# Performance work log

Measured on AMD Instinct MI355X. Metric: run time of the kernel, lower is better.

## Reference

```python
import jax, jax.numpy as jnp
import numpy as np

B, H, S, D = 4, 16, 2048, 64


def setup_inputs() -> dict:
    key = jax.random.key(0)
    kq, kk, kv = jax.random.split(key, 3)
    Q = jax.random.normal(kq, (B, H, S, D), dtype=jnp.float32)
    K = jax.random.normal(kk, (B, H, S, D), dtype=jnp.float32)
    V = jax.random.normal(kv, (B, H, S, D), dtype=jnp.float32)
    # causal mask, broadcasts over (B, H); True = keep, False (==0) = mask out
    mask = jnp.tril(jnp.ones((S, S), dtype=bool))
    return {"Q": Q, "K": K, "V": V, "mask": mask}


def reference(Q, K, V, mask):
    d_k = Q.shape[-1]
    scale = 1.0 / jnp.sqrt(jnp.asarray(d_k, dtype=Q.dtype))
    # [B,H,Sq,Sk] score matrix (the module materializes this fully)
    scores = jnp.einsum('bhqd,bhkd->bhqk', Q, K) * scale
    if mask is not None:
        scores = jnp.where(mask, scores, -jnp.inf)
    attn = jax.nn.softmax(scores, axis=-1)
    return jnp.einsum('bhqk,bhkd->bhqd', attn, V)
```

## Files before the change

kernel.cpp:

```cpp
#include <hip/hip_runtime.h>
#include <math.h>

namespace {

constexpr int SEQ   = 2048;
constexpr int DH    = 64;
constexpr int KVBLK = 64;
constexpr int QW    = 32;
constexpr int NWAVE = 4;
constexpr int QBLK  = QW * NWAVE;
constexpr int NQB   = SEQ / QBLK;
constexpr int BH    = 64;
constexpr int PADB  = 72;

typedef __bf16 bf16x8 __attribute__((ext_vector_type(8)));
typedef float  f32x16 __attribute__((ext_vector_type(16)));

union FragB { bf16x8 v; unsigned u[4]; __bf16 h[8]; };

__device__ __forceinline__ unsigned pack2(float a, float b) {
  unsigned r;
  asm("v_cvt_pk_bf16_f32 %0, %1, %2" : "=v"(r) : "v"(a), "v"(b));
  return r;
}

__device__ __forceinline__ void swap32(int a, int b, int &x, int &y) {
#if __has_builtin(__builtin_amdgcn_permlane32_swap)
  auto r = __builtin_amdgcn_permlane32_swap(a, b, false, false);
  x = r[0]; y = r[1];
#else
  const bool hi = ((threadIdx.x & 63) >= 32);
  const int sa = __shfl_xor(a, 32), sb = __shfl_xor(b, 32);
  x = hi ? sb : a;
  y = hi ? b  : sa;
#endif
}

__device__ __forceinline__ float xhalf_sum(float v) {
  int x, y; swap32(__float_as_int(v), __float_as_int(v), x, y);
  return __int_as_float(x) + __int_as_float(y);
}

__global__ __launch_bounds__(256, 2)
void attn_fwd(const float* __restrict__ Qg, const float* __restrict__ Kg,
              const float* __restrict__ Vg, float* __restrict__ Og)
{
  const int b   = blockIdx.x;
  const int j   = b >> 6;
  const int g   = j >> 2, k = j & 3;
  const int qi  = (g == 0) ? 15 - 2*k
                : (g == 1) ? 2*k
                : (g == 2) ? 14 - 2*k
                :            1 + 2*k;
  const int bh  = (b & 7) + 8 * ((b >> 3) & 7);
  const int qb  = qi * QBLK;
  const int qb64 = qb >> 6;

  const int tid  = threadIdx.x;
  const int wv   = tid >> 6;
  const int lane = tid & 63;
  const int l31  = lane & 31;
  const int hi   = lane >> 5;

  const size_t base = (size_t)bh * SEQ * DH;
  const float* Qp = Qg + base;
  const float* Kp = Kg + base;
  const float* Vp = Vg + base;
  float*       Op = Og + base;

  __shared__ __align__(16) unsigned char smem[36864];
  auto K_lds  = reinterpret_cast<__bf16(*)[KVBLK][PADB]>(smem);
  auto Vt_lds = reinterpret_cast<__bf16(*)[DH][PADB]>(smem + 18432);

  const float qscale = 0.125f * 1.44269504088896f;
  FragB bq[4];
  const int wq0 = wv * QW;
  {
    const float* src = Qp + (size_t)(qb + wq0 + l31) * DH + hi*8;
#pragma unroll
    for (int ks = 0; ks < 4; ++ks) {
      float4 f0 = *(const float4*)(src + ks*16);
      float4 f1 = *(const float4*)(src + ks*16 + 4);
      FragB f;
      f.u[0] = pack2(f0.x*qscale, f0.y*qscale);
      f.u[1] = pack2(f0.z*qscale, f0.w*qscale);
      f.u[2] = pack2(f1.x*qscale, f1.y*qscale);
      f.u[3] = pack2(f1.z*qscale, f1.w*qscale);
      bq[ks] = f;
    }
  }

  float4 kr[2][2];
  float  vr[16];
  const int kc8 = tid & 7;
  const int vd  = tid & 63;
  const int vk0 = (tid >> 6) * 16;

  auto load_tile = [&](int t) {
    const int kvb = t * KVBLK;
#pragma unroll
    for (int p = 0; p < 2; ++p) {
      const float* s = Kp + (size_t)(kvb + 32*p + (tid >> 3)) * DH + kc8*8;
      kr[p][0] = *(const float4*)s;
      kr[p][1] = *(const float4*)(s + 4);
    }
#pragma unroll
    for (int r = 0; r < 16; ++r)
      vr[r] = Vp[(size_t)(kvb + vk0 + r) * DH + vd];
  };

  auto store_tile = [&](int buf) {
#pragma unroll
    for (int p = 0; p < 2; ++p) {
      uint4 w;
      w.x = pack2(kr[p][0].x, kr[p][0].y); w.y = pack2(kr[p][0].z, kr[p][0].w);
      w.z = pack2(kr[p][1].x, kr[p][1].y); w.w = pack2(kr[p][1].z, kr[p][1].w);
      *reinterpret_cast<uint4*>(&K_lds[buf][32*p + (tid >> 3)][kc8*8]) = w;
    }
    uint4 w0, w1;
    w0.x = pack2(vr[0],  vr[1]);  w0.y = pack2(vr[2],  vr[3]);
    w0.z = pack2(vr[4],  vr[5]);  w0.w = pack2(vr[6],  vr[7]);
    w1.x = pack2(vr[8],  vr[9]);  w1.y = pack2(vr[10], vr[11]);
    w1.z = pack2(vr[12], vr[13]); w1.w = pack2(vr[14], vr[15]);
    *reinterpret_cast<uint4*>(&Vt_lds[buf][vd][vk0])     = w0;
    *reinterpret_cast<uint4*>(&Vt_lds[buf][vd][vk0 + 8]) = w1;
  };

  f32x16 oacc[2];
#pragma unroll
  for (int dt = 0; dt < 2; ++dt)
#pragma unroll
    for (int r = 0; r < 16; ++r) oacc[dt][r] = 0.f;
  float lpart = 0.f;

  const int NT = qb64 + 2;
  const int tmax_wave = qb64 + (wv >> 1);
  const int qloc = (wv & 1) * 32 + l31;

  load_tile(0);
  store_tile(0);
  __syncthreads();

  for (int t = 0; t < NT; ++t) {
    const int cur = t & 1;
    if (t + 1 < NT) load_tile(t + 1);

    if (t <= tmax_wave) {
      const bool diag = (t == tmax_wave);

      f32x16 st[2];
#pragma unroll
      for (int T = 0; T < 2; ++T)
#pragma unroll
        for (int r = 0; r < 16; ++r) st[T][r] = 0.f;
      __builtin_amdgcn_s_setprio(1);
#pragma unroll
      for (int T = 0; T < 2; ++T)
#pragma unroll
        for (int ks = 0; ks < 4; ++ks) {
          bf16x8 ak = *(const bf16x8*)&K_lds[cur][T*32 + l31][ks*16 + hi*8];
          st[T] = __builtin_amdgcn_mfma_f32_32x32x16_bf16(ak, bq[ks].v, st[T], 0, 0, 0);
        }
      __builtin_amdgcn_s_setprio(0);

      float p[2][16];
#pragma unroll
      for (int T = 0; T < 2; ++T)
#pragma unroll
        for (int r = 0; r < 16; ++r) {
          float s = st[T][r];
          if (diag) {
            const int kvl = T*32 + (r & 3) + 4*hi + 8*(r >> 2);
            if (kvl > qloc) s = -INFINITY;
          }
          const float e = exp2f(s);
          p[T][r] = e;
          lpart += e;
        }

      unsigned pk[2][8];
#pragma unroll
      for (int T = 0; T < 2; ++T)
#pragma unroll
        for (int j2 = 0; j2 < 8; ++j2) pk[T][j2] = pack2(p[T][2*j2], p[T][2*j2 + 1]);

      FragB pa[4];
#pragma unroll
      for (int ks = 0; ks < 4; ++ks) {
        const int T  = ks >> 1;
        const int gA = (2*ks) & 3;
        const int gB = (2*ks + 1) & 3;
        int x0, y0, x1, y1;
        swap32((int)pk[T][2*gA],     (int)pk[T][2*gB],     x0, y0);
        swap32((int)pk[T][2*gA + 1], (int)pk[T][2*gB + 1], x1, y1);
        pa[ks].u[0] = (unsigned)x0;
        pa[ks].u[1] = (unsigned)x1;
        pa[ks].u[2] = (unsigned)y0;
        pa[ks].u[3] = (unsigned)y1;
      }

      __builtin_amdgcn_s_setprio(1);
#pragma unroll
      for (int dt = 0; dt < 2; ++dt)
#pragma unroll
        for (int ks = 0; ks < 4; ++ks) {
          bf16x8 av = *(const bf16x8*)&Vt_lds[cur][dt*32 + l31][ks*16 + hi*8];
          oacc[dt] = __builtin_amdgcn_mfma_f32_32x32x16_bf16(av, pa[ks].v, oacc[dt], 0, 0, 0);
        }
      __builtin_amdgcn_s_setprio(0);
    }

    if (t + 1 < NT) store_tile(cur ^ 1);
    __syncthreads();
  }

  const float linv = 1.0f / xhalf_sum(lpart);
  float* slab = reinterpret_cast<float*>(smem) + wv * (QW * 68);

#pragma unroll
  for (int dt = 0; dt < 2; ++dt)
#pragma unroll
    for (int g2 = 0; g2 < 4; ++g2) {
      float4 w;
      w.x = oacc[dt][4*g2 + 0] * linv;
      w.y = oacc[dt][4*g2 + 1] * linv;
      w.z = oacc[dt][4*g2 + 2] * linv;
      w.w = oacc[dt][4*g2 + 3] * linv;
      *(float4*)&slab[l31*68 + dt*32 + 8*g2 + 4*hi] = w;
    }
  __syncthreads();
  {
    float* dst = Op + (size_t)(qb + wq0) * DH;
#pragma unroll
    for (int i = 0; i < 8; ++i) {
      const int row = i*4 + (lane >> 4);
      const int ch  = lane & 15;
      float4 v = *(const float4*)&slab[row*68 + ch*4];
      *(float4*)&dst[(size_t)row*DH + ch*4] = v;
    }
  }
}

}

extern "C" void kernel_launch(void* const* d_in, const int* in_sizes, int n_in,
                              void* d_out, int out_size, void* d_ws, size_t ws_size,
                              hipStream_t stream) {
  const float* Q = (const float*)d_in[0];
  const float* K = (const float*)d_in[1];
  const float* V = (const float*)d_in[2];
  float* O = (float*)d_out;
  attn_fwd<<<dim3(NQB * BH), dim3(256), 0, stream>>>(Q, K, V, O);
}
```

Before: 85.78 us.

## Pair complementary 64-row query blocks per workgroup and split KV across waves

Each workgroup now processes two 64-row query blocks (m and 31-m), giving every block exactly 33 KV tiles so the causal workload is balanced. Within a block, waves split the 64-key tile into two 32-key halves rather than each owning 32 query rows. The two partial output accumulators and row sums are merged through LDS before normalisation and store. Per-wave MFMA work per tile is halved, at the cost of an extra LDS reduction, extra barriers per query block, and a reload of Q mid-loop.

Result: slower. 101.6 us (+18.4%).

```diff
diff --git a/kernel.cpp b/kernel.cpp
--- a/kernel.cpp
+++ b/kernel.cpp
@@ -6,17 +6,13 @@
 constexpr int SEQ   = 2048;
 constexpr int DH    = 64;
 constexpr int KVBLK = 64;
-constexpr int QW    = 32;
-constexpr int NWAVE = 4;
-constexpr int QBLK  = QW * NWAVE;
-constexpr int NQB   = SEQ / QBLK;
 constexpr int BH    = 64;
 constexpr int PADB  = 72;
 
 typedef __bf16 bf16x8 __attribute__((ext_vector_type(8)));
 typedef float  f32x16 __attribute__((ext_vector_type(16)));
 
-union FragB { bf16x8 v; unsigned u[4]; __bf16 h[8]; };
+union FragB { bf16x8 v; unsigned u[4]; };
 
 __device__ __forceinline__ unsigned pack2(float a, float b) {
   unsigned r;
@@ -46,21 +42,20 @@
               const float* __restrict__ Vg, float* __restrict__ Og)
 {
   const int b   = blockIdx.x;
-  const int j   = b >> 6;
-  const int g   = j >> 2, k = j & 3;
-  const int qi  = (g == 0) ? 15 - 2*k
-                : (g == 1) ? 2*k
-                : (g == 2) ? 14 - 2*k
-                :            1 + 2*k;
-  const int bh  = (b & 7) + 8 * ((b >> 3) & 7);
-  const int qb  = qi * QBLK;
-  const int qb64 = qb >> 6;
+  const int bh  = b & 63;
+  const int m   = b >> 6;
+  const int qA  = 31 - m;
+  const int qB  = m;
+  const int NT  = 33;
 
   const int tid  = threadIdx.x;
   const int wv   = tid >> 6;
+  const int rw   = wv & 1;
+  const int kh   = wv >> 1;
   const int lane = tid & 63;
   const int l31  = lane & 31;
   const int hi   = lane >> 5;
+  const int qloc = rw * 32 + l31;
 
   const size_t base = (size_t)bh * SEQ * DH;
   const float* Qp = Qg + base;
@@ -74,21 +69,20 @@
 
   const float qscale = 0.125f * 1.44269504088896f;
   FragB bq[4];
-  const int wq0 = wv * QW;
-  {
-    const float* src = Qp + (size_t)(qb + wq0 + l31) * DH + hi*8;
+  auto load_q = [&](int qblk) {
+    const float* src = Qp + (size_t)(qblk*64 + rw*32 + l31) * DH + hi*8;
 #pragma unroll
     for (int ks = 0; ks < 4; ++ks) {
       float4 f0 = *(const float4*)(src + ks*16);
       float4 f1 = *(const float4*)(src + ks*16 + 4);
-      FragB f;
-      f.u[0] = pack2(f0.x*qscale, f0.y*qscale);
-      f.u[1] = pack2(f0.z*qscale, f0.w*qscale);
-      f.u[2] = pack2(f1.x*qscale, f1.y*qscale);
-      f.u[3] = pack2(f1.z*qscale, f1.w*qscale);
-      bq[ks] = f;
-    }
-  }
+      bq[ks].u[0] = pack2(f0.x*qscale, f0.y*qscale);
+      bq[ks].u[1] = pack2(f0.z*qscale, f0.w*qscale);
+      bq[ks].u[2] = pack2(f1.x*qscale, f1.y*qscale);
+      bq[ks].u[3] = pack2(f1.z*qscale, f1.w*qscale);
+    }
+  };
+  int qcur = qA;
+  load_q(qcur);
 
   float4 kr[2][2];
   float  vr[16];
@@ -96,8 +90,8 @@
   const int vd  = tid & 63;
   const int vk0 = (tid >> 6) * 16;
 
-  auto load_tile = [&](int t) {
-    const int kvb = t * KVBLK;
+  auto load_tile = [&](int tile) {
+    const int kvb = tile * KVBLK;
 #pragma unroll
     for (int p = 0; p < 2; ++p) {
       const float* s = Kp + (size_t)(kvb + 32*p + (tid >> 3)) * DH + kc8*8;
@@ -133,9 +127,7 @@
     for (int r = 0; r < 16; ++r) oacc[dt][r] = 0.f;
   float lpart = 0.f;
 
-  const int NT = qb64 + 2;
-  const int tmax_wave = qb64 + (wv >> 1);
-  const int qloc = (wv & 1) * 32 + l31;
+  auto tile_of = [&](int t) { return (t <= qA) ? t : t - (qA + 1); };
 
   load_tile(0);
   store_tile(0);
@@ -143,100 +135,123 @@
 
   for (int t = 0; t < NT; ++t) {
     const int cur = t & 1;
-    if (t + 1 < NT) load_tile(t + 1);
-
-    if (t <= tmax_wave) {
-      const bool diag = (t == tmax_wave);
-
-      f32x16 st[2];
-#pragma unroll
-      for (int T = 0; T < 2; ++T)
-#pragma unroll
-        for (int r = 0; r < 16; ++r) st[T][r] = 0.f;
-      __builtin_amdgcn_s_setprio(1);
-#pragma unroll
-      for (int T = 0; T < 2; ++T)
-#pragma unroll
-        for (int ks = 0; ks < 4; ++ks) {
-          bf16x8 ak = *(const bf16x8*)&K_lds[cur][T*32 + l31][ks*16 + hi*8];
-          st[T] = __builtin_amdgcn_mfma_f32_32x32x16_bf16(ak, bq[ks].v, st[T], 0, 0, 0);
-        }
-      __builtin_amdgcn_s_setprio(0);
-
-      float p[2][16];
-#pragma unroll
-      for (int T = 0; T < 2; ++T)
-#pragma unroll
-        for (int r = 0; r < 16; ++r) {
-          float s = st[T][r];
-          if (diag) {
-            const int kvl = T*32 + (r & 3) + 4*hi + 8*(r >> 2);
-            if (kvl > qloc) s = -INFINITY;
-          }
-          const float e = exp2f(s);
-          p[T][r] = e;
-          lpart += e;
-        }
-
-      unsigned pk[2][8];
-#pragma unroll
-      for (int T = 0; T < 2; ++T)
-#pragma unroll
-        for (int j2 = 0; j2 < 8; ++j2) pk[T][j2] = pack2(p[T][2*j2], p[T][2*j2 + 1]);
-
-      FragB pa[4];
-#pragma unroll
-      for (int ks = 0; ks < 4; ++ks) {
-        const int T  = ks >> 1;
-        const int gA = (2*ks) & 3;
-        const int gB = (2*ks + 1) & 3;
-        int x0, y0, x1, y1;
-        swap32((int)pk[T][2*gA],     (int)pk[T][2*gB],     x0, y0);
-        swap32((int)pk[T][2*gA + 1], (int)pk[T][2*gB + 1], x1, y1);
-        pa[ks].u[0] = (unsigned)x0;
-        pa[ks].u[1] = (unsigned)x1;
-        pa[ks].u[2] = (unsigned)y0;
-        pa[ks].u[3] = (unsigned)y1;
-      }
-
-      __builtin_amdgcn_s_setprio(1);
-#pragma unroll
-      for (int dt = 0; dt < 2; ++dt)
-#pragma unroll
-        for (int ks = 0; ks < 4; ++ks) {
-          bf16x8 av = *(const bf16x8*)&Vt_lds[cur][dt*32 + l31][ks*16 + hi*8];
-          oacc[dt] = __builtin_amdgcn_mfma_f32_32x32x16_bf16(av, pa[ks].v, oacc[dt], 0, 0, 0);
-        }
-      __builtin_amdgcn_s_setprio(0);
-    }
+    if (t + 1 < NT) load_tile(tile_of(t + 1));
+
+    const int  ts   = tile_of(t);
+    const bool diag = (ts == qcur);
+
+    f32x16 st;
+#pragma unroll
+    for (int r = 0; r < 16; ++r) st[r] = 0.f;
+    __builtin_amdgcn_s_setprio(1);
+#pragma unroll
+    for (int ks = 0; ks < 4; ++ks) {
+      bf16x8 ak = *(const bf16x8*)&K_lds[cur][kh*32 + l31][ks*16 + hi*8];
+      st = __builtin_amdgcn_mfma_f32_32x32x16_bf16(ak, bq[ks].v, st, 0, 0, 0);
+    }
+    __builtin_amdgcn_s_setprio(0);
+
+    float p[16];
+#pragma unroll
+    for (int r = 0; r < 16; ++r) {
+      float s = st[r];
+      if (diag) {
+        const int kvl = kh*32 + (r & 3) + 4*hi + 8*(r >> 2);
+        if (kvl > qloc) s = -INFINITY;
+      }
+      const float e = exp2f(s);
+      p[r] = e;
+      lpart += e;
+    }
+
+    unsigned pk[8];
+#pragma unroll
+    for (int j2 = 0; j2 < 8; ++j2) pk[j2] = pack2(p[2*j2], p[2*j2 + 1]);
+
+    FragB pa[2];
+#pragma unroll
+    for (int ks2 = 0; ks2 < 2; ++ks2) {
+      const int gA = 2*ks2, gB = 2*ks2 + 1;
+      int x0, y0, x1, y1;
+      swap32((int)pk[2*gA],     (int)pk[2*gB],     x0, y0);
+      swap32((int)pk[2*gA + 1], (int)pk[2*gB + 1], x1, y1);
+      pa[ks2].u[0] = (unsigned)x0;
+      pa[ks2].u[1] = (unsigned)x1;
+      pa[ks2].u[2] = (unsigned)y0;
+      pa[ks2].u[3] = (unsigned)y1;
+    }
+
+    __builtin_amdgcn_s_setprio(1);
+#pragma unroll
+    for (int dt = 0; dt < 2; ++dt)
+#pragma unroll
+      for (int ks2 = 0; ks2 < 2; ++ks2) {
+        bf16x8 av = *(const bf16x8*)&Vt_lds[cur][dt*32 + l31][kh*32 + ks2*16 + hi*8];
+        oacc[dt] = __builtin_amdgcn_mfma_f32_32x32x16_bf16(av, pa[ks2].v, oacc[dt], 0, 0, 0);
+      }
+    __builtin_amdgcn_s_setprio(0);
 
     if (t + 1 < NT) store_tile(cur ^ 1);
     __syncthreads();
-  }
-
-  const float linv = 1.0f / xhalf_sum(lpart);
-  float* slab = reinterpret_cast<float*>(smem) + wv * (QW * 68);
-
-#pragma unroll
-  for (int dt = 0; dt < 2; ++dt)
-#pragma unroll
-    for (int g2 = 0; g2 < 4; ++g2) {
-      float4 w;
-      w.x = oacc[dt][4*g2 + 0] * linv;
-      w.y = oacc[dt][4*g2 + 1] * linv;
-      w.z = oacc[dt][4*g2 + 2] * linv;
-      w.w = oacc[dt][4*g2 + 3] * linv;
-      *(float4*)&slab[l31*68 + dt*32 + 8*g2 + 4*hi] = w;
-    }
-  __syncthreads();
-  {
-    float* dst = Op + (size_t)(qb + wq0) * DH;
-#pragma unroll
-    for (int i = 0; i < 8; ++i) {
-      const int row = i*4 + (lane >> 4);
-      const int ch  = lane & 15;
-      float4 v = *(const float4*)&slab[row*68 + ch*4];
-      *(float4*)&dst[(size_t)row*DH + ch*4] = v;
+
+    if (t == qA || t == NT - 1) {
+      float* reg0 = reinterpret_cast<float*>(&K_lds[cur][0][0]);
+      float* reg1 = reinterpret_cast<float*>(&Vt_lds[cur][0][0]);
+      float* myreg = rw ? reg1 : reg0;
+      const int rb = l31 * 68;
+
+      if (kh == 1) {
+#pragma unroll
+        for (int dt = 0; dt < 2; ++dt)
+#pragma unroll
+          for (int g4 = 0; g4 < 4; ++g4) {
+            float4 w;
+            w.x = oacc[dt][4*g4 + 0]; w.y = oacc[dt][4*g4 + 1];
+            w.z = oacc[dt][4*g4 + 2]; w.w = oacc[dt][4*g4 + 3];
+            *(float4*)&myreg[rb + dt*32 + 8*g4 + 4*hi] = w;
+          }
+        const float s1 = xhalf_sum(lpart);
+        if (hi == 0) myreg[rb + 64] = s1;
+      }
+      __syncthreads();
+      if (kh == 0) {
+        const float linv = 1.0f / (xhalf_sum(lpart) + myreg[rb + 64]);
+#pragma unroll
+        for (int dt = 0; dt < 2; ++dt)
+#pragma unroll
+          for (int g4 = 0; g4 < 4; ++g4) {
+            float4 v = *(const float4*)&myreg[rb + dt*32 + 8*g4 + 4*hi];
+            v.x = (v.x + oacc[dt][4*g4 + 0]) * linv;
+            v.y = (v.y + oacc[dt][4*g4 + 1]) * linv;
+            v.z = (v.z + oacc[dt][4*g4 + 2]) * linv;
+            v.w = (v.w + oacc[dt][4*g4 + 3]) * linv;
+            *(float4*)&myreg[rb + dt*32 + 8*g4 + 4*hi] = v;
+          }
+      }
+      __syncthreads();
+      {
+        float* dst = Op + (size_t)(qcur * 64) * DH;
+#pragma unroll
+        for (int i = 0; i < 4; ++i) {
+          const int f   = tid + i*256;
+          const int row = f >> 4;
+          const int ch  = f & 15;
+          const float* srcrow = (row < 32) ? (reg0 + row*68) : (reg1 + (row-32)*68);
+          float4 v = *(const float4*)&srcrow[ch*4];
+          *(float4*)&dst[(size_t)row*DH + ch*4] = v;
+        }
+      }
+      __syncthreads();
+
+      if (t != NT - 1) {
+        qcur = qB;
+#pragma unroll
+        for (int dt = 0; dt < 2; ++dt)
+#pragma unroll
+          for (int r = 0; r < 16; ++r) oacc[dt][r] = 0.f;
+        lpart = 0.f;
+        load_q(qcur);
+      }
     }
   }
 }
@@ -250,5 +265,5 @@
   const float* K = (const float*)d_in[1];
   const float* V = (const float*)d_in[2];
   float* O = (float*)d_out;
-  attn_fwd<<<dim3(NQB * BH), dim3(256), 0, stream>>>(Q, K, V, O);
-}
+  attn_fwd<<<dim3(16 * BH), dim3(256), 0, stream>>>(Q, K, V, O);
+}
```
